# Optimization experiments

Measured on AMD Instinct MI355X. Metric: run time of the kernel, lower is better.

Reference implementation:

```python
import jax, jax.numpy as jnp
import numpy as np

N_EXPERTS = 16
IN_DIM = 1024
OUT_DIM = 1024
BATCH = 4096

def setup_inputs() -> dict:
    key = jax.random.key(0)
    k1, k2, k3, k4 = jax.random.split(key, 4)
    x = jax.random.normal(k1, (BATCH, IN_DIM), dtype=jnp.float32)
    comp_weight = jax.random.uniform(k2, (BATCH, N_EXPERTS), dtype=jnp.float32)
    # torch.rand init (uniform [0,1)) per original module
    weight = jax.random.uniform(k3, (N_EXPERTS, IN_DIM, OUT_DIM), dtype=jnp.float32)
    bias = jax.random.uniform(k4, (N_EXPERTS, OUT_DIM), dtype=jnp.float32)
    return {"x": x, "comp_weight": comp_weight, "weight": weight, "bias": bias}

def reference(x, comp_weight, weight, bias):
    # z[n,b,o] = x[b,i] @ weight[n,i,o] + bias[n,o]   (baddbmm)
    z = jnp.einsum('bi,nio->nbo', x, weight) + bias[:, None, :]
    # out[b,o] = sum_n comp_weight[b,n] * z[n,b,o]    (bmm combine)
    out = jnp.einsum('bn,nbo->bo', comp_weight, z)
    return jax.nn.relu(out)
```

## Files before the change

kernel.cpp:

```cpp
#include <hip/hip_runtime.h>
#include <hip/hip_bf16.h>
#include <cstdint>

#define BATCH   4096
#define IN_DIM  1024
#define OUT_DIM 1024
#define NEXP    16

typedef __bf16 bf16;
typedef __attribute__((ext_vector_type(8))) __bf16 bf16x8;
typedef __attribute__((ext_vector_type(4))) float  f32x4;

#define AS1 __attribute__((address_space(1)))
#define AS3 __attribute__((address_space(3)))

__device__ __forceinline__ void gld_lds16(const bf16* g, bf16* l) {
    __builtin_amdgcn_global_load_lds((const AS1 void*)g, (AS3 void*)l, 16, 0, 0);
}

__global__ void convert_x_tiled(const float* __restrict__ x, bf16* __restrict__ xt) {
    int tile = blockIdx.x;
    int mblk = tile >> 4, ks = tile & 15;
    int t = threadIdx.x;
#pragma unroll
    for (int r = 0; r < 4; r++) {
        int q = r * 256 + t;
        int m_loc = q >> 3, sc = q & 7;
        int c = sc ^ (m_loc & 7);
        const float* src = x + (size_t)(mblk * 128 + m_loc) * IN_DIM + ks * 64 + c * 8;
        f32x4 a = *(const f32x4*)src;
        f32x4 b = *(const f32x4*)(src + 4);
        bf16x8 v;
#pragma unroll
        for (int j = 0; j < 4; j++) { v[j] = (bf16)a[j]; v[4 + j] = (bf16)b[j]; }
        *(bf16x8*)(xt + (size_t)tile * 8192 + q * 8) = v;
    }
}

__global__ void convert_w_frag(const float* __restrict__ W, bf16* __restrict__ wt) {
    int tile = blockIdx.x;
    int nblk = tile >> 8, ne = (tile >> 4) & 15, ks = tile & 15;
    int t = threadIdx.x;
#pragma unroll
    for (int r = 0; r < 2; r++) {
        int c = r * 256 + t;
        int sub = c >> 6, l = c & 63;
        int lr = l & 15, lq = l >> 4;
        int kk = sub >> 2, wn = (sub >> 1) & 1, nt = sub & 1;
        int kbase = ne * 1024 + ks * 64 + kk * 32 + lq * 8;
        int ng = nblk * 64 + wn * 32 + nt * 16 + lr;
        bf16x8 v;
#pragma unroll
        for (int j = 0; j < 8; j++)
            v[j] = (bf16)W[(size_t)(kbase + j) * OUT_DIM + ng];
        *(bf16x8*)(wt + (size_t)tile * 4096 + c * 8) = v;
    }
}

__global__ __launch_bounds__(256, 3) void moe_gemm(
        const float* __restrict__ cw, const float* __restrict__ bias,
        const bf16* __restrict__ xt, const bf16* __restrict__ wt,
        float* __restrict__ out) {
    int nblk = blockIdx.x;
    int mblk = blockIdx.y;
    int m0 = mblk * 128, n0 = nblk * 64;
    int t = threadIdx.x;
    int lane = t & 63, w = t >> 6;
    int wm = w >> 1, wn = w & 1;
    int lq = lane >> 4, lr = lane & 15;

    __shared__ bf16 As[128 * 64];
    __shared__ bf16 Bs[2][64 * 64];
    __shared__ float cwT[16 * 132];

#pragma unroll
    for (int r = 0; r < 2; r++) {
        int q = r * 256 + t;
        f32x4 v = *(const f32x4*)(cw + (size_t)m0 * NEXP + q * 4);
        int row = q >> 2, nb = (q & 3) * 4;
#pragma unroll
        for (int c2 = 0; c2 < 4; c2++) cwT[(nb + c2) * 132 + row] = v[c2];
    }

    const f32x4 fz = {0.f, 0.f, 0.f, 0.f};
    f32x4 acc[4][2];
#pragma unroll
    for (int mt = 0; mt < 4; mt++)
#pragma unroll
        for (int nt = 0; nt < 2; nt++) acc[mt][nt] = fz;

    int swz = lr & 7;
    int mrow[4];
#pragma unroll
    for (int mt = 0; mt < 4; mt++) mrow[mt] = (wm * 64 + mt * 16 + lr) * 64;

    const bf16* abase = xt + (size_t)(mblk * 16) * 8192;
    const bf16* bbase = wt + (size_t)nblk * (16 * 16 * 4096);

    for (int ks = 0; ks < 16; ks++) {
        const bf16* asrc = abase + (size_t)ks * 8192 + t * 8;
#pragma unroll
        for (int r = 0; r < 4; r++) gld_lds16(asrc + r * 2048, &As[r * 2048 + t * 8]);
        const bf16* b0 = bbase + (size_t)ks * 4096 + t * 8;
#pragma unroll
        for (int r = 0; r < 2; r++) gld_lds16(b0 + r * 2048, &Bs[0][r * 2048 + t * 8]);
        __syncthreads();

        bf16x8 af[4][2];
#pragma unroll
        for (int kk = 0; kk < 2; kk++)
#pragma unroll
            for (int mt = 0; mt < 4; mt++)
                af[mt][kk] = *(const bf16x8*)&As[mrow[mt] + ((kk * 4 + lq) ^ swz) * 8];

#pragma unroll 2
        for (int ne = 0; ne < NEXP; ne++) {
            int buf = ne & 1;
            if (ne < 15) {
                const bf16* bn = bbase + (size_t)((ne + 1) * 16 + ks) * 4096 + t * 8;
#pragma unroll
                for (int r = 0; r < 2; r++)
                    gld_lds16(bn + r * 2048, &Bs[buf ^ 1][r * 2048 + t * 8]);
            }
            bf16x8 bfr[2][2];
#pragma unroll
            for (int kk = 0; kk < 2; kk++)
#pragma unroll
                for (int nt = 0; nt < 2; nt++)
                    bfr[kk][nt] = *(const bf16x8*)
                        &Bs[buf][((kk * 2 + wn) * 2 + nt) * 512 + lane * 8];
            f32x4 s[4];
#pragma unroll
            for (int mt = 0; mt < 4; mt++)
                s[mt] = *(const f32x4*)&cwT[ne * 132 + wm * 64 + mt * 16 + lq * 4];
#pragma unroll
            for (int mt = 0; mt < 4; mt++)
#pragma unroll
                for (int nt = 0; nt < 2; nt++) {
                    f32x4 p = __builtin_amdgcn_mfma_f32_16x16x32_bf16(
                        af[mt][0], bfr[0][nt], fz, 0, 0, 0);
                    p = __builtin_amdgcn_mfma_f32_16x16x32_bf16(
                        af[mt][1], bfr[1][nt], p, 0, 0, 0);
                    acc[mt][nt] += s[mt] * p;
                }
            __syncthreads();
        }
    }

    {
        bf16x8 acw[4];
#pragma unroll
        for (int mt = 0; mt < 4; mt++) {
            bf16x8 v;
#pragma unroll
            for (int j = 0; j < 8; j++) v[j] = (bf16)0.f;
            if (lq < 2) {
                int row = m0 + wm * 64 + mt * 16 + lr;
                f32x4 a = *(const f32x4*)(cw + (size_t)row * NEXP + lq * 8);
                f32x4 b = *(const f32x4*)(cw + (size_t)row * NEXP + lq * 8 + 4);
#pragma unroll
                for (int j = 0; j < 4; j++) { v[j] = (bf16)a[j]; v[4 + j] = (bf16)b[j]; }
            }
            acw[mt] = v;
        }
        bf16x8 bb[2];
#pragma unroll
        for (int nt = 0; nt < 2; nt++) {
            bf16x8 v;
#pragma unroll
            for (int j = 0; j < 8; j++) v[j] = (bf16)0.f;
            if (lq < 2) {
                int col = n0 + wn * 32 + nt * 16 + lr;
#pragma unroll
                for (int j = 0; j < 8; j++)
                    v[j] = (bf16)bias[(size_t)(lq * 8 + j) * OUT_DIM + col];
            }
            bb[nt] = v;
        }
#pragma unroll
        for (int mt = 0; mt < 4; mt++)
#pragma unroll
            for (int nt = 0; nt < 2; nt++)
                acc[mt][nt] = __builtin_amdgcn_mfma_f32_16x16x32_bf16(
                    acw[mt], bb[nt], acc[mt][nt], 0, 0, 0);
    }

#pragma unroll
    for (int mt = 0; mt < 4; mt++) {
        int row = m0 + wm * 64 + mt * 16 + lq * 4;
#pragma unroll
        for (int nt = 0; nt < 2; nt++) {
            int col = n0 + wn * 32 + nt * 16 + lr;
#pragma unroll
            for (int r2 = 0; r2 < 4; r2++) {
                float v = acc[mt][nt][r2];
                out[(size_t)(row + r2) * OUT_DIM + col] = v > 0.f ? v : 0.f;
            }
        }
    }
}

__global__ void fallback_kernel(const float* __restrict__ x, const float* __restrict__ cw,
                                const float* __restrict__ W, const float* __restrict__ bias,
                                float* __restrict__ out) {
    int o = blockIdx.x * 256 + threadIdx.x;
    int b = o >> 10, oc = o & 1023;
    const float* xr = x + (size_t)b * IN_DIM;
    float accv = 0.f;
    for (int n = 0; n < NEXP; n++) {
        const float* wr = W + (size_t)n * IN_DIM * OUT_DIM + oc;
        float z = 0.f;
        for (int i = 0; i < IN_DIM; i++) z += xr[i] * wr[(size_t)i * OUT_DIM];
        accv += cw[(size_t)b * NEXP + n] * (z + bias[n * OUT_DIM + oc]);
    }
    out[o] = accv > 0.f ? accv : 0.f;
}

extern "C" void kernel_launch(void* const* d_in, const int* in_sizes, int n_in,
                              void* d_out, int out_size, void* d_ws, size_t ws_size,
                              hipStream_t stream) {
    const float* x    = (const float*)d_in[0];
    const float* cw   = (const float*)d_in[1];
    const float* W    = (const float*)d_in[2];
    const float* bias = (const float*)d_in[3];
    float* out = (float*)d_out;

    const size_t wt_elems = (size_t)NEXP * IN_DIM * OUT_DIM;
    const size_t xt_elems = (size_t)BATCH * IN_DIM;
    if (ws_size < (wt_elems + xt_elems) * sizeof(bf16)) {
        fallback_kernel<<<(BATCH * OUT_DIM) / 256, 256, 0, stream>>>(x, cw, W, bias, out);
        return;
    }
    bf16* wt = (bf16*)d_ws;
    bf16* xt = wt + wt_elems;

    convert_w_frag<<<4096, 256, 0, stream>>>(W, wt);
    convert_x_tiled<<<512, 256, 0, stream>>>(x, xt);
    moe_gemm<<<dim3(16, 32), 256, 0, stream>>>(cw, bias, xt, wt, out);
}
```

Measured before the change: 256.2 us.

## Transpose MoE GEMM roles, read W fragments directly, fuse conversion kernels

The two conversion kernels become one launch, and W is now transposed through shared memory so its global reads are coalesced instead of strided. The main GEMM swaps operand roles so weights are the MFMA A operand and x the B operand. Weight fragments are read straight from global memory rather than staged in LDS, which drops the per-expert __syncthreads, and x tiles are double-buffered in LDS. Output is written as f32x4 vectors and comp_weight is read from global, with the risk of higher global/L2 latency on the weight loads.

```diff
diff --git a/kernel.cpp b/kernel.cpp
--- a/kernel.cpp
+++ b/kernel.cpp
@@ -18,184 +18,186 @@
     __builtin_amdgcn_global_load_lds((const AS1 void*)g, (AS3 void*)l, 16, 0, 0);
 }
 
-__global__ void convert_x_tiled(const float* __restrict__ x, bf16* __restrict__ xt) {
-    int tile = blockIdx.x;
-    int mblk = tile >> 4, ks = tile & 15;
+__global__ void pre_convert(const float* __restrict__ x, const float* __restrict__ W,
+                            bf16* __restrict__ xt, bf16* __restrict__ wt2) {
+    __shared__ float lt[64][68];
     int t = threadIdx.x;
-#pragma unroll
-    for (int r = 0; r < 4; r++) {
-        int q = r * 256 + t;
-        int m_loc = q >> 3, sc = q & 7;
-        int c = sc ^ (m_loc & 7);
-        const float* src = x + (size_t)(mblk * 128 + m_loc) * IN_DIM + ks * 64 + c * 8;
-        f32x4 a = *(const f32x4*)src;
-        f32x4 b = *(const f32x4*)(src + 4);
-        bf16x8 v;
-#pragma unroll
-        for (int j = 0; j < 4; j++) { v[j] = (bf16)a[j]; v[4 + j] = (bf16)b[j]; }
-        *(bf16x8*)(xt + (size_t)tile * 8192 + q * 8) = v;
-    }
-}
-
-__global__ void convert_w_frag(const float* __restrict__ W, bf16* __restrict__ wt) {
-    int tile = blockIdx.x;
-    int nblk = tile >> 8, ne = (tile >> 4) & 15, ks = tile & 15;
-    int t = threadIdx.x;
-#pragma unroll
-    for (int r = 0; r < 2; r++) {
-        int c = r * 256 + t;
-        int sub = c >> 6, l = c & 63;
-        int lr = l & 15, lq = l >> 4;
-        int kk = sub >> 2, wn = (sub >> 1) & 1, nt = sub & 1;
-        int kbase = ne * 1024 + ks * 64 + kk * 32 + lq * 8;
-        int ng = nblk * 64 + wn * 32 + nt * 16 + lr;
-        bf16x8 v;
-#pragma unroll
-        for (int j = 0; j < 8; j++)
-            v[j] = (bf16)W[(size_t)(kbase + j) * OUT_DIM + ng];
-        *(bf16x8*)(wt + (size_t)tile * 4096 + c * 8) = v;
-    }
-}
-
-__global__ __launch_bounds__(256, 3) void moe_gemm(
+    if (blockIdx.x < 512) {
+        int tile = blockIdx.x;
+        int bblk = tile >> 4, ks = tile & 15;
+#pragma unroll
+        for (int r = 0; r < 4; r++) {
+            int q = r * 256 + t;
+            int b_loc = q >> 3, sc = q & 7;
+            int c = sc ^ (b_loc & 7);
+            const float* src = x + (size_t)(bblk * 128 + b_loc) * IN_DIM + ks * 64 + c * 8;
+            f32x4 a = *(const f32x4*)src;
+            f32x4 b = *(const f32x4*)(src + 4);
+            bf16x8 v;
+#pragma unroll
+            for (int j = 0; j < 4; j++) { v[j] = (bf16)a[j]; v[4 + j] = (bf16)b[j]; }
+            *(bf16x8*)(xt + (size_t)tile * 8192 + q * 8) = v;
+        }
+    } else {
+        int t2 = blockIdx.x - 512;
+        int oblk = t2 >> 8, ne = (t2 >> 4) & 15, ks = t2 & 15;
+        int kbase = ne * 1024 + ks * 64, o0 = oblk * 64;
+#pragma unroll
+        for (int r = 0; r < 4; r++) {
+            int q = r * 256 + t;
+            int row = q >> 4, cg = q & 15;
+            f32x4 v = *(const f32x4*)(W + (size_t)(kbase + row) * OUT_DIM + o0 + cg * 4);
+#pragma unroll
+            for (int c = 0; c < 4; c++) lt[row][cg * 4 + c] = v[c];
+        }
+        __syncthreads();
+#pragma unroll
+        for (int r = 0; r < 2; r++) {
+            int c = r * 256 + t;
+            int sub = c >> 6, l = c & 63;
+            int lr = l & 15, lq = l >> 4;
+            int kk = sub >> 2, wm = (sub >> 1) & 1, mt = sub & 1;
+            int o_loc = wm * 32 + mt * 16 + lr;
+            int kb2 = kk * 32 + lq * 8;
+            bf16x8 v;
+#pragma unroll
+            for (int j = 0; j < 8; j++) v[j] = (bf16)lt[kb2 + j][o_loc];
+            *(bf16x8*)(wt2 + (size_t)t2 * 4096 + c * 8) = v;
+        }
+    }
+}
+
+__global__ __launch_bounds__(256, 3) void moe_gemm_t(
         const float* __restrict__ cw, const float* __restrict__ bias,
-        const bf16* __restrict__ xt, const bf16* __restrict__ wt,
+        const bf16* __restrict__ xt, const bf16* __restrict__ wt2,
         float* __restrict__ out) {
-    int nblk = blockIdx.x;
-    int mblk = blockIdx.y;
-    int m0 = mblk * 128, n0 = nblk * 64;
+    int bblk = blockIdx.x;
+    int oblk = blockIdx.y;
+    int b0 = bblk * 128, o0 = oblk * 64;
     int t = threadIdx.x;
     int lane = t & 63, w = t >> 6;
-    int wm = w >> 1, wn = w & 1;
+    int wm = w & 1, wb = w >> 1;
     int lq = lane >> 4, lr = lane & 15;
-
-    __shared__ bf16 As[128 * 64];
-    __shared__ bf16 Bs[2][64 * 64];
-    __shared__ float cwT[16 * 132];
-
-#pragma unroll
-    for (int r = 0; r < 2; r++) {
-        int q = r * 256 + t;
-        f32x4 v = *(const f32x4*)(cw + (size_t)m0 * NEXP + q * 4);
-        int row = q >> 2, nb = (q & 3) * 4;
-#pragma unroll
-        for (int c2 = 0; c2 < 4; c2++) cwT[(nb + c2) * 132 + row] = v[c2];
-    }
+    int swz = lr & 7;
+
+    __shared__ bf16 As[2][128 * 64];
 
     const f32x4 fz = {0.f, 0.f, 0.f, 0.f};
-    f32x4 acc[4][2];
-#pragma unroll
-    for (int mt = 0; mt < 4; mt++)
-#pragma unroll
-        for (int nt = 0; nt < 2; nt++) acc[mt][nt] = fz;
-
-    int swz = lr & 7;
-    int mrow[4];
-#pragma unroll
-    for (int mt = 0; mt < 4; mt++) mrow[mt] = (wm * 64 + mt * 16 + lr) * 64;
-
-    const bf16* abase = xt + (size_t)(mblk * 16) * 8192;
-    const bf16* bbase = wt + (size_t)nblk * (16 * 16 * 4096);
+    f32x4 acc[2][4];
+#pragma unroll
+    for (int mt = 0; mt < 2; mt++)
+#pragma unroll
+        for (int bt = 0; bt < 4; bt++) acc[mt][bt] = fz;
+
+    int brow[4];
+#pragma unroll
+    for (int bt = 0; bt < 4; bt++) brow[bt] = (wb * 64 + bt * 16 + lr) * 64;
+
+    const bf16* xtile = xt + (size_t)(bblk * 16) * 8192;
+    const bf16* wtile = wt2 + (size_t)(oblk * 256) * 4096;
+    const float* cwl = cw + (size_t)(b0 + wb * 64 + lr) * NEXP;
+
+#pragma unroll
+    for (int r = 0; r < 4; r++)
+        gld_lds16(xtile + r * 2048 + t * 8, &As[0][r * 2048 + t * 8]);
 
     for (int ks = 0; ks < 16; ks++) {
-        const bf16* asrc = abase + (size_t)ks * 8192 + t * 8;
-#pragma unroll
-        for (int r = 0; r < 4; r++) gld_lds16(asrc + r * 2048, &As[r * 2048 + t * 8]);
-        const bf16* b0 = bbase + (size_t)ks * 4096 + t * 8;
-#pragma unroll
-        for (int r = 0; r < 2; r++) gld_lds16(b0 + r * 2048, &Bs[0][r * 2048 + t * 8]);
         __syncthreads();
-
-        bf16x8 af[4][2];
+        if (ks < 15) {
+            const bf16* nx = xtile + (size_t)(ks + 1) * 8192 + t * 8;
+#pragma unroll
+            for (int r = 0; r < 4; r++)
+                gld_lds16(nx + r * 2048, &As[(ks + 1) & 1][r * 2048 + t * 8]);
+        }
+        bf16x8 xf[2][4];
 #pragma unroll
         for (int kk = 0; kk < 2; kk++)
 #pragma unroll
-            for (int mt = 0; mt < 4; mt++)
-                af[mt][kk] = *(const bf16x8*)&As[mrow[mt] + ((kk * 4 + lq) ^ swz) * 8];
-
+            for (int bt = 0; bt < 4; bt++)
+                xf[kk][bt] = *(const bf16x8*)
+                    &As[ks & 1][brow[bt] + ((kk * 4 + lq) ^ swz) * 8];
+
+        const bf16* wks = wtile + (size_t)ks * 4096;
 #pragma unroll 2
-        for (int ne = 0; ne < NEXP; ne++) {
-            int buf = ne & 1;
-            if (ne < 15) {
-                const bf16* bn = bbase + (size_t)((ne + 1) * 16 + ks) * 4096 + t * 8;
-#pragma unroll
-                for (int r = 0; r < 2; r++)
-                    gld_lds16(bn + r * 2048, &Bs[buf ^ 1][r * 2048 + t * 8]);
+        for (int g = 0; g < 4; g++) {
+            f32x4 sc[4];
+#pragma unroll
+            for (int bt = 0; bt < 4; bt++)
+                sc[bt] = *(const f32x4*)(cwl + bt * 16 * NEXP + g * 4);
+#pragma unroll
+            for (int j2 = 0; j2 < 4; j2++) {
+                int ne = g * 4 + j2;
+                const bf16* wp = wks + (size_t)ne * (16 * 4096);
+                bf16x8 wf[2][2];
+#pragma unroll
+                for (int kk = 0; kk < 2; kk++)
+#pragma unroll
+                    for (int mt = 0; mt < 2; mt++)
+                        wf[kk][mt] = *(const bf16x8*)
+                            (wp + ((kk * 4 + wm * 2 + mt) * 64 + lane) * 8);
+#pragma unroll
+                for (int mt = 0; mt < 2; mt++)
+#pragma unroll
+                    for (int bt = 0; bt < 4; bt++) {
+                        f32x4 p = __builtin_amdgcn_mfma_f32_16x16x32_bf16(
+                            wf[0][mt], xf[0][bt], fz, 0, 0, 0);
+                        p = __builtin_amdgcn_mfma_f32_16x16x32_bf16(
+                            wf[1][mt], xf[1][bt], p, 0, 0, 0);
+                        float s = sc[bt][j2];
+                        acc[mt][bt] += s * p;
+                    }
             }
-            bf16x8 bfr[2][2];
-#pragma unroll
-            for (int kk = 0; kk < 2; kk++)
-#pragma unroll
-                for (int nt = 0; nt < 2; nt++)
-                    bfr[kk][nt] = *(const bf16x8*)
-                        &Bs[buf][((kk * 2 + wn) * 2 + nt) * 512 + lane * 8];
-            f32x4 s[4];
-#pragma unroll
-            for (int mt = 0; mt < 4; mt++)
-                s[mt] = *(const f32x4*)&cwT[ne * 132 + wm * 64 + mt * 16 + lq * 4];
-#pragma unroll
-            for (int mt = 0; mt < 4; mt++)
-#pragma unroll
-                for (int nt = 0; nt < 2; nt++) {
-                    f32x4 p = __builtin_amdgcn_mfma_f32_16x16x32_bf16(
-                        af[mt][0], bfr[0][nt], fz, 0, 0, 0);
-                    p = __builtin_amdgcn_mfma_f32_16x16x32_bf16(
-                        af[mt][1], bfr[1][nt], p, 0, 0, 0);
-                    acc[mt][nt] += s[mt] * p;
-                }
-            __syncthreads();
         }
     }
 
     {
-        bf16x8 acw[4];
-#pragma unroll
-        for (int mt = 0; mt < 4; mt++) {
+        bf16x8 bfrag[2];
+#pragma unroll
+        for (int mt = 0; mt < 2; mt++) {
             bf16x8 v;
 #pragma unroll
             for (int j = 0; j < 8; j++) v[j] = (bf16)0.f;
             if (lq < 2) {
-                int row = m0 + wm * 64 + mt * 16 + lr;
-                f32x4 a = *(const f32x4*)(cw + (size_t)row * NEXP + lq * 8);
-                f32x4 b = *(const f32x4*)(cw + (size_t)row * NEXP + lq * 8 + 4);
+                int og = o0 + wm * 32 + mt * 16 + lr;
+#pragma unroll
+                for (int j = 0; j < 8; j++)
+                    v[j] = (bf16)bias[(size_t)(lq * 8 + j) * OUT_DIM + og];
+            }
+            bfrag[mt] = v;
+        }
+        bf16x8 cwf[4];
+#pragma unroll
+        for (int bt = 0; bt < 4; bt++) {
+            bf16x8 v;
+#pragma unroll
+            for (int j = 0; j < 8; j++) v[j] = (bf16)0.f;
+            if (lq < 2) {
+                const float* cr = cwl + bt * 16 * NEXP + lq * 8;
+                f32x4 a = *(const f32x4*)cr;
+                f32x4 b = *(const f32x4*)(cr + 4);
 #pragma unroll
                 for (int j = 0; j < 4; j++) { v[j] = (bf16)a[j]; v[4 + j] = (bf16)b[j]; }
             }
-            acw[mt] = v;
-        }
-        bf16x8 bb[2];
-#pragma unroll
-        for (int nt = 0; nt < 2; nt++) {
-            bf16x8 v;
-#pragma unroll
-            for (int j = 0; j < 8; j++) v[j] = (bf16)0.f;
-            if (lq < 2) {
-                int col = n0 + wn * 32 + nt * 16 + lr;
-#pragma unroll
-                for (int j = 0; j < 8; j++)
-                    v[j] = (bf16)bias[(size_t)(lq * 8 + j) * OUT_DIM + col];
-            }
-            bb[nt] = v;
-        }
-#pragma unroll
-        for (int mt = 0; mt < 4; mt++)
-#pragma unroll
-            for (int nt = 0; nt < 2; nt++)
-                acc[mt][nt] = __builtin_amdgcn_mfma_f32_16x16x32_bf16(
-                    acw[mt], bb[nt], acc[mt][nt], 0, 0, 0);
-    }
-
-#pragma unroll
-    for (int mt = 0; mt < 4; mt++) {
-        int row = m0 + wm * 64 + mt * 16 + lq * 4;
-#pragma unroll
-        for (int nt = 0; nt < 2; nt++) {
-            int col = n0 + wn * 32 + nt * 16 + lr;
-#pragma unroll
-            for (int r2 = 0; r2 < 4; r2++) {
-                float v = acc[mt][nt][r2];
-                out[(size_t)(row + r2) * OUT_DIM + col] = v > 0.f ? v : 0.f;
-            }
+            cwf[bt] = v;
+        }
+#pragma unroll
+        for (int mt = 0; mt < 2; mt++)
+#pragma unroll
+            for (int bt = 0; bt < 4; bt++)
+                acc[mt][bt] = __builtin_amdgcn_mfma_f32_16x16x32_bf16(
+                    bfrag[mt], cwf[bt], acc[mt][bt], 0, 0, 0);
+    }
+
+#pragma unroll
+    for (int mt = 0; mt < 2; mt++) {
+        int og = o0 + wm * 32 + mt * 16 + lq * 4;
+#pragma unroll
+        for (int bt = 0; bt < 4; bt++) {
+            int bg = b0 + wb * 64 + bt * 16 + lr;
+            f32x4 v = acc[mt][bt];
+#pragma unroll
+            for (int r2 = 0; r2 < 4; r2++) v[r2] = v[r2] > 0.f ? v[r2] : 0.f;
+            *(f32x4*)(out + (size_t)bg * OUT_DIM + og) = v;
         }
     }
 }
@@ -231,10 +233,9 @@
         fallback_kernel<<<(BATCH * OUT_DIM) / 256, 256, 0, stream>>>(x, cw, W, bias, out);
         return;
     }
-    bf16* wt = (bf16*)d_ws;
-    bf16* xt = wt + wt_elems;
-
-    convert_w_frag<<<4096, 256, 0, stream>>>(W, wt);
-    convert_x_tiled<<<512, 256, 0, stream>>>(x, xt);
-    moe_gemm<<<dim3(16, 32), 256, 0, stream>>>(cw, bias, xt, wt, out);
-}
+    bf16* wt2 = (bf16*)d_ws;
+    bf16* xt = wt2 + wt_elems;
+
+    pre_convert<<<4608, 256, 0, stream>>>(x, W, xt, wt2);
+    moe_gemm_t<<<dim3(32, 16), 256, 0, stream>>>(cw, bias, xt, wt2, out);
+}
```

Result: slower. 329.8 us (+28.7%).
